# Kernel tuning notes

Hardware: AMD Instinct MI355X
Metric: run time of the kernel (lower is better)

Reference implementation:

```python
import jax, jax.numpy as jnp
import numpy as np

B, L, S, H, E = 2, 2048, 2048, 16, 64


def setup_inputs() -> dict:
    key = jax.random.key(0)
    kq, kk, kv = jax.random.split(key, 3)
    queries = jax.random.normal(kq, (B, L, H, E), dtype=jnp.float32)
    keys = jax.random.normal(kk, (B, S, H, E), dtype=jnp.float32)
    values = jax.random.normal(kv, (B, S, H, E), dtype=jnp.float32)
    attn_mask = jnp.ones((B, 1, L, S), dtype=jnp.float32)  # >0.5 means attend
    return {"queries": queries, "keys": keys, "values": values, "attn_mask": attn_mask}


def reference(queries, keys, values, attn_mask):
    # queries: [B,L,H,E], keys/values: [B,S,H,E], attn_mask broadcastable to [B,H,L,S]
    E_ = queries.shape[-1]
    scale = 1.0 / np.sqrt(E_).astype(np.float32)
    scores = jnp.einsum('blhe,bshe->bhls', queries, keys)  # [B,H,L,S]
    large_negative = jnp.float32(-1e9)
    scores = scores + jnp.where(attn_mask > 0.5, jnp.float32(0.0), large_negative)
    A = jax.nn.softmax(scale * scores, axis=-1)  # dropout p=0.0 -> identity
    V = jnp.einsum('bhls,bshd->bhld', A, values)  # [B,H,L,D]
    return V
```

## Files before the change

kernel.cpp:

```cpp
#include <hip/hip_runtime.h>

typedef float    f32x4 __attribute__((ext_vector_type(4)));
typedef _Float16 f16x2 __attribute__((ext_vector_type(2)));
typedef _Float16 f16x4 __attribute__((ext_vector_type(4)));
typedef _Float16 f16x8 __attribute__((ext_vector_type(8)));
typedef int      i32x4 __attribute__((ext_vector_type(4)));

namespace {
constexpr int B_ = 2, L_ = 2048, S_ = 2048, H_ = 16, E_ = 64;
constexpr int MBLK = 128;
constexpr int NT = 64;
constexpr int NTILES = S_ / NT;

#define SCALE2f 0.1803368801111204f
#define MBIAS2f -1.8033688e8f

constexpr size_t KHOFF = (size_t)1 << 20;
constexpr size_t VHOFF = KHOFF + (size_t)B_ * H_ * S_ * E_ * 2;

__device__ __forceinline__ f16x2 cvt2(float a, float b) {
  return __builtin_bit_cast(f16x2, __builtin_amdgcn_cvt_pkrtz(a, b));
}
__device__ __forceinline__ int pkh(float a, float b) {
  return __builtin_bit_cast(int, __builtin_amdgcn_cvt_pkrtz(a, b));
}
union H8 { f16x8 v; i32x4 i; };
union H4 { f16x4 v; f16x2 h[2]; };

#define GLOAD_LDS16(g, l)                                              \
  __builtin_amdgcn_global_load_lds(                                    \
      (const __attribute__((address_space(1))) void*)(g),              \
      (__attribute__((address_space(3))) void*)(l), 16, 0, 0)
}

extern "C" __global__ __launch_bounds__(256)
void prep_kernel(const float* __restrict__ Kg, const float* __restrict__ Vg,
                 const float* __restrict__ Mg, _Float16* __restrict__ Kh,
                 _Float16* __restrict__ Vh, unsigned long long* __restrict__ Wb) {
  __shared__ _Float16 T[64][72];
  const int bid = blockIdx.x;
  const int t   = threadIdx.x;

  if (bid < 2048) {
    const int idx = bid * 256 + t;
    const int j = idx & 7;
    const int h = (idx >> 3) & (H_ - 1);
    const int s = (idx >> 7) & (S_ - 1);
    const int b = idx >> 18;
    const float* src = Kg + ((((size_t)b * S_ + s) * H_ + h) << 6) + j * 8;
    f32x4 x = *(const f32x4*)src, y = *(const f32x4*)(src + 4);
    i32x4 w = {pkh(x[0], x[1]), pkh(x[2], x[3]), pkh(y[0], y[1]), pkh(y[2], y[3])};
    *(i32x4*)(Kh + ((((size_t)b * H_ + h) * S_ + s) << 6) + j * 8) = w;
  } else if (bid < 4096) {
    const int u = (bid - 2048) * 256 + t;
    const float* src = Mg + (size_t)u * 16;
    unsigned m = 0;
#pragma unroll
    for (int i = 0; i < 4; ++i) {
      f32x4 x = *(const f32x4*)(src + i * 4);
#pragma unroll
      for (int c = 0; c < 4; ++c) m |= (x[c] > 0.5f ? 1u : 0u) << (i * 4 + c);
    }
    ((unsigned short*)Wb)[u] = (unsigned short)m;
  } else {
    const int vb = bid - 4096;
    const int st = vb & 31;
    const int h  = (vb >> 5) & (H_ - 1);
    const int b  = vb >> 9;
    const int sl = t >> 2;
    const int e0 = (t & 3) << 4;
    const float* src = Vg + ((((size_t)b * S_ + st * 64 + sl) * H_ + h) << 6) + e0;
#pragma unroll
    for (int i = 0; i < 4; ++i) {
      f32x4 x = *(const f32x4*)(src + i * 4);
#pragma unroll
      for (int c = 0; c < 4; ++c) T[e0 + i * 4 + c][sl] = (_Float16)x[c];
    }
    __syncthreads();
    const int er = t >> 2;
    const int s0 = (t & 3) << 4;
    _Float16* dst = Vh + (((((size_t)b * H_ + h) << 6) + er) * S_) + st * 64 + s0;
    *(i32x4*)dst       = *(const i32x4*)&T[er][s0];
    *(i32x4*)(dst + 8) = *(const i32x4*)&T[er][s0 + 8];
  }
}

extern "C" __global__ __launch_bounds__(256, 2)
void fattn_kernel(const float* __restrict__ Qg, const _Float16* __restrict__ Kh,
                  const _Float16* __restrict__ Vh, const unsigned long long* __restrict__ Wb,
                  float* __restrict__ Og) {
  __shared__ __align__(16) _Float16 Ks[3][NT][64];
  __shared__ __align__(16) _Float16 Vt[3][E_][64];

  const int tid  = threadIdx.x;
  const int wv   = tid >> 6;
  const int lane = tid & 63;
  const int qd   = lane >> 4;
  const int cl   = lane & 15;
  const int sw   = cl & 7;

  const int bid = blockIdx.x;
  const int qb  = bid >> 5;
  const int bh  = bid & 31;
  const int h   = bh & (H_ - 1);
  const int b   = bh >> 4;

  const int l0 = qb * MBLK + wv * 32;

  f16x8 qf[2][2];
#pragma unroll
  for (int mt = 0; mt < 2; ++mt) {
    const float* qp = Qg + ((((size_t)b * L_ + (l0 + mt * 16 + cl)) * H_ + h) << 6);
#pragma unroll
    for (int kb = 0; kb < 2; ++kb) {
      const int e0 = qd * 8 + kb * 32;
      f32x4 x = *(const f32x4*)(qp + e0);
      f32x4 y = *(const f32x4*)(qp + e0 + 4);
      x *= SCALE2f;
      y *= SCALE2f;
      H8 u;
      u.i = (i32x4){pkh(x[0], x[1]), pkh(x[2], x[3]), pkh(y[0], y[1]), pkh(y[2], y[3])};
      qf[mt][kb] = u.v;
    }
  }

  const int rl  = lane >> 3;
  const int gsl = lane & 7;
  const int gsw = gsl ^ rl;
  const _Float16* khb = Kh + ((((size_t)b * H_ + h) * S_) << 6);
  const _Float16* vhb = Vh + ((((size_t)b * H_ + h) << 6) * (size_t)S_);

  const unsigned long long* wbp = Wb + (((size_t)b * L_ + (l0 + cl)) << 5);

  auto dma = [&](int buf, int t) {
#pragma unroll
    for (int p = 0; p < 2; ++p) {
      const int r0 = p * 32 + wv * 8;
      const _Float16* ksrc = khb + (((size_t)(t * 64 + r0 + rl)) << 6) + gsw * 8;
      GLOAD_LDS16(ksrc, &Ks[buf][r0][0]);
      const _Float16* vsrc = vhb + (size_t)(r0 + rl) * S_ + t * 64 + gsw * 8;
      GLOAD_LDS16(vsrc, &Vt[buf][r0][0]);
    }
  };

  const f32x4 zero4 = {0.f, 0.f, 0.f, 0.f};
  f32x4 acc[2][4];
#pragma unroll
  for (int mt = 0; mt < 2; ++mt)
#pragma unroll
    for (int et = 0; et < 4; ++et) acc[mt][et] = zero4;
  f32x4 rs4[2] = {zero4, zero4};

  unsigned long long mwcur = wbp[0];
  dma(0, 0);
  asm volatile("" ::: "memory");
  unsigned long long mwnext = wbp[1];
  dma(1, 1);
  asm volatile("" ::: "memory");

  int bc = 0;
  for (int t = 0; t < NTILES; ++t) {
    if (t < NTILES - 1)
      asm volatile("s_waitcnt vmcnt(5)" ::: "memory");
    else
      asm volatile("s_waitcnt vmcnt(0)" ::: "memory");
    __builtin_amdgcn_s_barrier();

    unsigned long long mwnext2 = 0;
    const int bn = (bc == 2) ? 0 : bc + 1;
    if (t + 2 < NTILES) {
      const int b2 = (bn == 2) ? 0 : bn + 1;
      mwnext2 = wbp[t + 2];
      dma(b2, t + 2);
    }
    asm volatile("" ::: "memory");

    f32x4 sc[4][2];
#pragma unroll
    for (int nt = 0; nt < 4; ++nt) {
      const _Float16* krow = &Ks[bc][nt * 16 + cl][0];
      const f16x8 a0 = *(const f16x8*)(krow + ((qd ^ sw) << 3));
      const f16x8 a1 = *(const f16x8*)(krow + (((qd + 4) ^ sw) << 3));
#pragma unroll
      for (int mt = 0; mt < 2; ++mt) {
        f32x4 c = zero4;
        c = __builtin_amdgcn_mfma_f32_16x16x32_f16(a0, qf[mt][0], c, 0, 0, 0);
        c = __builtin_amdgcn_mfma_f32_16x16x32_f16(a1, qf[mt][1], c, 0, 0, 0);
        sc[nt][mt] = c;
      }
    }

    f16x4 pa[2][4];
    if (mwcur == ~0ull) {
#pragma unroll
      for (int mt = 0; mt < 2; ++mt)
#pragma unroll
        for (int nt = 0; nt < 4; ++nt) {
          f32x4 p;
#pragma unroll
          for (int r = 0; r < 4; ++r)
            p[r] = __builtin_amdgcn_exp2f(sc[nt][mt][r]);
          rs4[mt] += p;
          H4 u;
          u.h[0] = cvt2(p[0], p[1]);
          u.h[1] = cvt2(p[2], p[3]);
          pa[mt][nt] = u.v;
        }
    } else {
      const unsigned lo = (unsigned)mwcur;
      const unsigned hi = (unsigned)(mwcur >> 32);
#pragma unroll
      for (int mt = 0; mt < 2; ++mt)
#pragma unroll
        for (int nt = 0; nt < 4; ++nt) {
          const unsigned shm = ((nt < 2) ? lo : hi) >> ((nt & 1) * 16 + qd * 4);
          f32x4 p;
#pragma unroll
          for (int r = 0; r < 4; ++r) {
            const float bias = (shm & (1u << r)) ? 0.f : MBIAS2f;
            p[r] = __builtin_amdgcn_exp2f(sc[nt][mt][r] + bias);
          }
          rs4[mt] += p;
          H4 u;
          u.h[0] = cvt2(p[0], p[1]);
          u.h[1] = cvt2(p[2], p[3]);
          pa[mt][nt] = u.v;
        }
    }

#pragma unroll
    for (int nt = 0; nt < 4; ++nt)
#pragma unroll
      for (int et = 0; et < 4; ++et) {
        const _Float16* vrow = &Vt[bc][et * 16 + cl][0];
        const f16x4 bv = *(const f16x4*)(vrow + ((((2 * nt + (qd >> 1)) ^ sw) << 3) + ((qd & 1) << 2)));
        acc[0][et] = __builtin_amdgcn_mfma_f32_16x16x16f16(pa[0][nt], bv, acc[0][et], 0, 0, 0);
        acc[1][et] = __builtin_amdgcn_mfma_f32_16x16x16f16(pa[1][nt], bv, acc[1][et], 0, 0, 0);
      }

    mwcur = mwnext;
    mwnext = mwnext2;
    bc = bn;
  }

#pragma unroll
  for (int mt = 0; mt < 2; ++mt) {
    float v = rs4[mt][0] + rs4[mt][1] + rs4[mt][2] + rs4[mt][3];
    v += __shfl_xor(v, 16, 64);
    v += __shfl_xor(v, 32, 64);
#pragma unroll
    for (int r = 0; r < 4; ++r) {
      const float invq = 1.0f / __shfl(v, qd * 4 + r, 64);
      const int l = l0 + mt * 16 + qd * 4 + r;
      float* op = Og + ((((size_t)b * H_ + h) * L_ + l) << 6) + cl;
#pragma unroll
      for (int et = 0; et < 4; ++et) op[et * 16] = acc[mt][et][r] * invq;
    }
  }
}

extern "C" void kernel_launch(void* const* d_in, const int* in_sizes, int n_in,
                              void* d_out, int out_size, void* d_ws, size_t ws_size,
                              hipStream_t stream) {
  const float* Q = (const float*)d_in[0];
  const float* K = (const float*)d_in[1];
  const float* V = (const float*)d_in[2];
  const float* M = (const float*)d_in[3];
  float* O = (float*)d_out;
  unsigned long long* Wb = (unsigned long long*)d_ws;
  _Float16* Khp = (_Float16*)((char*)d_ws + KHOFF);
  _Float16* Vhp = (_Float16*)((char*)d_ws + VHOFF);

  hipLaunchKernelGGL(prep_kernel, dim3(5120), dim3(256), 0, stream, K, V, M, Khp, Vhp, Wb);
  hipLaunchKernelGGL(fattn_kernel, dim3(B_ * H_ * (L_ / MBLK)), dim3(256), 0, stream,
                     Q, Khp, Vhp, Wb, O);
}
```

Measured before the change: 163.8 us.

## Use 16x16x32 MFMA for PV product and ballot-based mask bit packing

The PV accumulation now packs pairs of 16-wide P fragments into 8-wide f16 vectors and issues 16x16x32 MFMAs, halving the number of matrix instructions per tile. Matching V fragments are built from two 4-element LDS reads. The mask prep now uses wave ballots to pack bits in a new layout, and the masked bias extraction in the attention loop is updated to read that layout. This reduces MFMA issue count and speeds up mask packing, but it depends on the new bit layout matching the MFMA lane mapping exactly.

```diff
diff --git a/kernel.cpp b/kernel.cpp
--- a/kernel.cpp
+++ b/kernel.cpp
@@ -24,7 +24,7 @@
 __device__ __forceinline__ int pkh(float a, float b) {
   return __builtin_bit_cast(int, __builtin_amdgcn_cvt_pkrtz(a, b));
 }
-union H8 { f16x8 v; i32x4 i; };
+union H8 { f16x8 v; i32x4 i; f16x4 h4[2]; };
 union H4 { f16x4 v; f16x2 h[2]; };
 
 #define GLOAD_LDS16(g, l)                                              \
@@ -52,16 +52,26 @@
     i32x4 w = {pkh(x[0], x[1]), pkh(x[2], x[3]), pkh(y[0], y[1]), pkh(y[2], y[3])};
     *(i32x4*)(Kh + ((((size_t)b * H_ + h) * S_ + s) << 6) + j * 8) = w;
   } else if (bid < 4096) {
-    const int u = (bid - 2048) * 256 + t;
-    const float* src = Mg + (size_t)u * 16;
-    unsigned m = 0;
-#pragma unroll
-    for (int i = 0; i < 4; ++i) {
-      f32x4 x = *(const f32x4*)(src + i * 4);
-#pragma unroll
-      for (int c = 0; c < 4; ++c) m |= (x[c] > 0.5f ? 1u : 0u) << (i * 4 + c);
-    }
-    ((unsigned short*)Wb)[u] = (unsigned short)m;
+    const int wv2   = t >> 6;
+    const int lane2 = t & 63;
+    const size_t wave_id = (size_t)(bid - 2048) * 4 + wv2;
+    const float* mp = Mg + wave_id * 1024 + lane2 * 4;
+    unsigned long long* wp = Wb + wave_id * 16;
+#pragma unroll
+    for (int k = 0; k < 4; ++k) {
+      const f32x4 x = *(const f32x4*)(mp + k * 256);
+      const unsigned long long b0 = __ballot(x[0] > 0.5f);
+      const unsigned long long b1 = __ballot(x[1] > 0.5f);
+      const unsigned long long b2 = __ballot(x[2] > 0.5f);
+      const unsigned long long b3 = __ballot(x[3] > 0.5f);
+      if (lane2 < 4) {
+        const int sh = lane2 * 16;
+        const unsigned long long w =
+            ((b0 >> sh) & 0xFFFFull) | (((b1 >> sh) & 0xFFFFull) << 16) |
+            (((b2 >> sh) & 0xFFFFull) << 32) | (((b3 >> sh) & 0xFFFFull) << 48);
+        wp[k * 4 + lane2] = w;
+      }
+    }
   } else {
     const int vb = bid - 4096;
     const int st = vb & 31;
@@ -190,7 +200,7 @@
       }
     }
 
-    f16x4 pa[2][4];
+    H8 pa8[2][2];
     if (mwcur == ~0ull) {
 #pragma unroll
       for (int mt = 0; mt < 2; ++mt)
@@ -204,7 +214,7 @@
           H4 u;
           u.h[0] = cvt2(p[0], p[1]);
           u.h[1] = cvt2(p[2], p[3]);
-          pa[mt][nt] = u.v;
+          pa8[mt][nt >> 1].h4[nt & 1] = u.v;
         }
     } else {
       const unsigned lo = (unsigned)mwcur;
@@ -213,29 +223,31 @@
       for (int mt = 0; mt < 2; ++mt)
 #pragma unroll
         for (int nt = 0; nt < 4; ++nt) {
-          const unsigned shm = ((nt < 2) ? lo : hi) >> ((nt & 1) * 16 + qd * 4);
+          const unsigned m0 = lo >> (4 * nt + qd);
+          const unsigned m1 = hi >> (4 * nt + qd);
           f32x4 p;
-#pragma unroll
-          for (int r = 0; r < 4; ++r) {
-            const float bias = (shm & (1u << r)) ? 0.f : MBIAS2f;
-            p[r] = __builtin_amdgcn_exp2f(sc[nt][mt][r] + bias);
-          }
+          p[0] = __builtin_amdgcn_exp2f(sc[nt][mt][0] + ((m0 & 1u)       ? 0.f : MBIAS2f));
+          p[1] = __builtin_amdgcn_exp2f(sc[nt][mt][1] + ((m0 & 0x10000u) ? 0.f : MBIAS2f));
+          p[2] = __builtin_amdgcn_exp2f(sc[nt][mt][2] + ((m1 & 1u)       ? 0.f : MBIAS2f));
+          p[3] = __builtin_amdgcn_exp2f(sc[nt][mt][3] + ((m1 & 0x10000u) ? 0.f : MBIAS2f));
           rs4[mt] += p;
           H4 u;
           u.h[0] = cvt2(p[0], p[1]);
           u.h[1] = cvt2(p[2], p[3]);
-          pa[mt][nt] = u.v;
+          pa8[mt][nt >> 1].h4[nt & 1] = u.v;
         }
     }
 
 #pragma unroll
-    for (int nt = 0; nt < 4; ++nt)
+    for (int ntp = 0; ntp < 2; ++ntp)
 #pragma unroll
       for (int et = 0; et < 4; ++et) {
         const _Float16* vrow = &Vt[bc][et * 16 + cl][0];
-        const f16x4 bv = *(const f16x4*)(vrow + ((((2 * nt + (qd >> 1)) ^ sw) << 3) + ((qd & 1) << 2)));
-        acc[0][et] = __builtin_amdgcn_mfma_f32_16x16x16f16(pa[0][nt], bv, acc[0][et], 0, 0, 0);
-        acc[1][et] = __builtin_amdgcn_mfma_f32_16x16x16f16(pa[1][nt], bv, acc[1][et], 0, 0, 0);
+        H8 bv;
+        bv.h4[0] = *(const f16x4*)(vrow + ((((ntp * 4 + (qd >> 1)) ^ sw) << 3) + ((qd & 1) << 2)));
+        bv.h4[1] = *(const f16x4*)(vrow + ((((ntp * 4 + 2 + (qd >> 1)) ^ sw) << 3) + ((qd & 1) << 2)));
+        acc[0][et] = __builtin_amdgcn_mfma_f32_16x16x32_f16(pa8[0][ntp].v, bv.v, acc[0][et], 0, 0, 0);
+        acc[1][et] = __builtin_amdgcn_mfma_f32_16x16x32_f16(pa8[1][ntp].v, bv.v, acc[1][et], 0, 0, 0);
       }
 
     mwcur = mwnext;
```

New measurement: 159.6 us. -2.6%, faster.
